# Kernel optimization log

Hardware: AMD Instinct MI355X
Metric: run time of the kernel (lower is better)

Reference implementation:

```python
import jax, jax.numpy as jnp
import numpy as np

SCALES = (16, 32, 64, 128)
P = 8
D = 1024
H = 16
DEPTH = 8
MLP = 4096
NCLS = 1000
PB = [(s // P) ** 2 for s in SCALES]            # [4, 16, 64, 256]
BLOCKS = [PB[0] + 1] + PB[1:]                    # [5, 16, 64, 256]
L = sum(BLOCKS)                                  # 341
PATCH_L = sum(PB)                                # 340
PD = P * P * 3                                   # 192
HD = D // H
EPS = 1e-6

# scale id per token (start token belongs to scale 0)
_SID = np.concatenate([np.full(n, k, dtype=np.int32) for k, n in enumerate(BLOCKS)])
# additive block-causal mask: token in scale q may attend to scales <= q
_ALLOW = _SID[None, :] <= _SID[:, None]
MASK = jnp.where(jnp.asarray(_ALLOW), 0.0, -1e30).astype(jnp.float32)  # [L, L]
SID = jnp.asarray(_SID)


def _ln(x):
    m = jnp.mean(x, axis=-1, keepdims=True)
    v = jnp.var(x, axis=-1, keepdims=True)
    return (x - m) / jnp.sqrt(v + EPS)


def _l2n(t):
    n = jnp.sqrt(jnp.sum(t * t, axis=-1, keepdims=True))
    return t / jnp.maximum(n, 1e-12)


def setup_inputs() -> dict:
    key = jax.random.key(0)
    ks = jax.random.split(key, 16)
    s = 0.02
    inp = {
        "patches": jax.random.normal(ks[0], (8, PATCH_L, PD), jnp.float32),
        "labels": jax.random.randint(ks[1], (8,), 0, NCLS),
        "W_patch": s * jax.random.normal(ks[2], (PD, D), jnp.float32),
        "b_patch": jnp.zeros((D,), jnp.float32),
        "pos": s * jax.random.normal(ks[3], (1, L, D), jnp.float32),
        "scale_emb": s * jax.random.normal(ks[4], (len(SCALES), D), jnp.float32),
        "class_emb": s * jax.random.normal(ks[5], (NCLS + 1, D), jnp.float32),
        "ada_W": s * jax.random.normal(ks[6], (DEPTH, D, 6 * D), jnp.float32),
        "ada_b": jnp.zeros((DEPTH, 6 * D), jnp.float32),
        "qkv_W": s * jax.random.normal(ks[7], (DEPTH, D, 3 * D), jnp.float32),
        "qkv_b": jnp.zeros((DEPTH, 3 * D), jnp.float32),
        "q_scale": jnp.zeros((DEPTH, 1, 1, H, 1), jnp.float32),  # log-scale per head
        "proj_W": s * jax.random.normal(ks[8], (DEPTH, D, D), jnp.float32),
        "proj_b": jnp.zeros((DEPTH, D), jnp.float32),
        "fc1_W": s * jax.random.normal(ks[9], (DEPTH, D, MLP), jnp.float32),
        "fc1_b": jnp.zeros((DEPTH, MLP), jnp.float32),
        "fc2_W": s * jax.random.normal(ks[10], (DEPTH, MLP, D), jnp.float32),
        "fc2_b": jnp.zeros((DEPTH, D), jnp.float32),
        "head_ada_W": s * jax.random.normal(ks[11], (D, 2 * D), jnp.float32),
        "head_ada_b": jnp.zeros((2 * D,), jnp.float32),
        "head_W": s * jax.random.normal(ks[12], (D, PD), jnp.float32),
        "head_b": jnp.zeros((PD,), jnp.float32),
    }
    return inp


def reference(patches, labels, W_patch, b_patch, pos, scale_emb, class_emb,
              ada_W, ada_b, qkv_W, qkv_b, q_scale, proj_W, proj_b,
              fc1_W, fc1_b, fc2_W, fc2_b, head_ada_W, head_ada_b, head_W, head_b):
    B = patches.shape[0]
    cond = class_emb[labels]                              # [B, D]
    tok = patches @ W_patch + b_patch                     # [B, PATCH_L, D]
    x = jnp.concatenate([cond[:, None, :], tok], axis=1)  # [B, L, D]
    x = x + pos + scale_emb[SID]

    for i in range(DEPTH):
        ada = jax.nn.silu(cond) @ ada_W[i] + ada_b[i]     # [B, 6D]
        g1, g2, s1, s2, sh1, sh2 = [a[:, None, :] for a in jnp.split(ada, 6, axis=-1)]
        # attention branch
        h = _ln(x) * (s1 + 1.0) + sh1
        qkv = (h @ qkv_W[i] + qkv_b[i]).reshape(B, L, 3, H, HD)
        q, k, v = qkv[:, :, 0], qkv[:, :, 1], qkv[:, :, 2]  # [B, L, H, HD]
        q = _l2n(q) * jnp.exp(q_scale[i])                  # attn_l2_norm
        k = _l2n(k)
        scores = jnp.einsum("bqhd,bkhd->bhqk", q, k) + MASK
        attn = jax.nn.softmax(scores, axis=-1)
        o = jnp.einsum("bhqk,bkhd->bqhd", attn, v).reshape(B, L, D)
        x = x + g1 * (o @ proj_W[i] + proj_b[i])
        # mlp branch
        h2 = _ln(x) * (s2 + 1.0) + sh2
        m = jax.nn.gelu(h2 @ fc1_W[i] + fc1_b[i]) @ fc2_W[i] + fc2_b[i]
        x = x + g2 * m

    ada = jax.nn.silu(cond) @ head_ada_W + head_ada_b     # [B, 2D]
    sc, sh = [a[:, None, :] for a in jnp.split(ada, 2, axis=-1)]
    x = _ln(x) * (sc + 1.0) + sh
    return x @ head_W + head_b                            # [B, L, PD]
```

## Files before the change

### kernel.cpp

```cpp
#include <hip/hip_runtime.h>

typedef unsigned short ushort_t;
typedef __bf16 bf16x8 __attribute__((ext_vector_type(8)));
typedef float f32x4 __attribute__((ext_vector_type(4)));

#define DEV __device__ __forceinline__

DEV ushort_t f2bf(float x) {
  union { float f; unsigned u; } v; v.f = x;
  unsigned r = v.u + 0x7FFFu + ((v.u >> 16) & 1u);
  return (ushort_t)(r >> 16);
}
DEV int sid_of(int l) { return l < 5 ? 0 : (l < 21 ? 1 : (l < 85 ? 2 : 3)); }
DEV float fast_tanh(float u) { return 1.0f - 2.0f / (__expf(2.0f * u) + 1.0f); }
DEV float gelu_f(float x) {
  float u = 0.7978845608028654f * (x + 0.044715f * x * x * x);
  return 0.5f * x * (1.0f + fast_tanh(u));
}
DEV float silu_f(float x) { return x / (1.0f + __expf(-x)); }
DEV f32x4 mfma16(bf16x8 a, bf16x8 b, f32x4 c) {
  return __builtin_amdgcn_mfma_f32_16x16x32_bf16(a, b, c, 0, 0, 0);
}
DEV void gload16(const void* src, void* dst) {
  __builtin_amdgcn_global_load_lds(
      (const __attribute__((address_space(1))) void*)(uintptr_t)src,
      (__attribute__((address_space(3))) void*)(uintptr_t)dst, 16, 0, 0);
}

__global__ __launch_bounds__(256) void k_cond_x0(
    const int* __restrict__ labels, const float* __restrict__ class_emb,
    const float* __restrict__ pos, const float* __restrict__ semb,
    float* __restrict__ cond, float* __restrict__ x) {
  int b = blockIdx.x, t = threadIdx.x;
  int lab = labels[b];
  float4 cv = *(const float4*)&class_emb[(size_t)lab * 1024 + t * 4];
  *(float4*)&cond[(size_t)b * 1024 + t * 4] = cv;
  float4 pv = *(const float4*)&pos[t * 4];
  float4 sv = *(const float4*)&semb[t * 4];
  float4 xv;
  xv.x = cv.x + pv.x + sv.x; xv.y = cv.y + pv.y + sv.y;
  xv.z = cv.z + pv.z + sv.z; xv.w = cv.w + pv.w + sv.w;
  *(float4*)&x[(size_t)b * 341 * 1024 + t * 4] = xv;
}

__global__ __launch_bounds__(256) void k_convert(const float* __restrict__ src,
                                                 ushort_t* __restrict__ dst, int n4) {
  int i = blockIdx.x * 256 + threadIdx.x;
  if (i < n4) {
    float4 v = *(const float4*)&src[(size_t)i * 4];
    uint2 pk;
    pk.x = (unsigned)f2bf(v.x) | ((unsigned)f2bf(v.y) << 16);
    pk.y = (unsigned)f2bf(v.z) | ((unsigned)f2bf(v.w) << 16);
    *(uint2*)&dst[(size_t)i * 4] = pk;
  }
}

__global__ __launch_bounds__(256) void k_transpose(const float* __restrict__ src,
                                                   ushort_t* __restrict__ dst, int K, int N) {
  __shared__ ushort_t tile[32][33];
  int z = blockIdx.z;
  src += (size_t)z * K * N;
  dst += (size_t)z * K * N;
  int k0 = blockIdx.y * 32, n0 = blockIdx.x * 32;
  int t = threadIdx.x;
  int r = t >> 3, c = (t & 7) * 4;
  float4 v = *(const float4*)&src[(size_t)(k0 + r) * N + n0 + c];
  tile[r][c] = f2bf(v.x); tile[r][c + 1] = f2bf(v.y);
  tile[r][c + 2] = f2bf(v.z); tile[r][c + 3] = f2bf(v.w);
  __syncthreads();
  ushort_t o0 = tile[c][r], o1 = tile[c + 1][r], o2 = tile[c + 2][r], o3 = tile[c + 3][r];
  uint2 pk;
  pk.x = (unsigned)o0 | ((unsigned)o1 << 16);
  pk.y = (unsigned)o2 | ((unsigned)o3 << 16);
  *(uint2*)&dst[(size_t)(n0 + r) * K + k0 + c] = pk;
}

__global__ __launch_bounds__(256) void k_ada(const float* __restrict__ cond,
    const float* __restrict__ ada_W, const float* __restrict__ ada_b,
    const float* __restrict__ hada_W, const float* __restrict__ hada_b,
    float* __restrict__ ada_out, float* __restrict__ hada_out) {
  int gy = blockIdx.y;
  bool head = (gy == 8);
  int Nw = head ? 2048 : 6144;
  int n0 = blockIdx.x * 64;
  if (n0 >= Nw) return;
  __shared__ float sc[8 * 1024];
  __shared__ float red[4][64][8];
  int t = threadIdx.x;
  for (int i = t; i < 2048; i += 256) {
    float4 cv = *(const float4*)&cond[(size_t)i * 4];
    float* d = &sc[i * 4];
    d[0] = silu_f(cv.x); d[1] = silu_f(cv.y); d[2] = silu_f(cv.z); d[3] = silu_f(cv.w);
  }
  __syncthreads();
  const float* W = head ? hada_W : ada_W + (size_t)gy * 1024 * 6144;
  const float* bs = head ? hada_b : ada_b + (size_t)gy * 6144;
  float* op = head ? hada_out : ada_out + (size_t)gy * 8 * 6144;
  int col = n0 + (t & 63), kq = t >> 6;
  float acc[8] = {0.f, 0.f, 0.f, 0.f, 0.f, 0.f, 0.f, 0.f};
  for (int k = kq * 256; k < kq * 256 + 256; ++k) {
    float wv = W[(size_t)k * Nw + col];
#pragma unroll
    for (int b2 = 0; b2 < 8; ++b2) acc[b2] += wv * sc[b2 * 1024 + k];
  }
#pragma unroll
  for (int b2 = 0; b2 < 8; ++b2) red[kq][t & 63][b2] = acc[b2];
  __syncthreads();
  if (t < 64) {
    int colc = n0 + t;
    float bias = bs[colc];
#pragma unroll
    for (int b2 = 0; b2 < 8; ++b2) {
      float v = red[0][t][b2] + red[1][t][b2] + red[2][t][b2] + red[3][t][b2] + bias;
      op[(size_t)b2 * Nw + colc] = v;
    }
  }
}

__global__ __launch_bounds__(256) void k_ln(const float* __restrict__ x,
    ushort_t* __restrict__ hout, const float* __restrict__ ada,
    int stride, int soff, int shoff) {
  int row = blockIdx.x, t = threadIdx.x;
  int b = row / 341;
  const float* xr = x + (size_t)row * 1024;
  float4 xv = *(const float4*)&xr[t * 4];
  float s = xv.x + xv.y + xv.z + xv.w;
  float ss = xv.x * xv.x + xv.y * xv.y + xv.z * xv.z + xv.w * xv.w;
#pragma unroll
  for (int off = 1; off < 64; off <<= 1) { s += __shfl_xor(s, off); ss += __shfl_xor(ss, off); }
  __shared__ float red[8];
  int w = t >> 6, lane = t & 63;
  if (lane == 0) { red[w] = s; red[w + 4] = ss; }
  __syncthreads();
  s = red[0] + red[1] + red[2] + red[3];
  ss = red[4] + red[5] + red[6] + red[7];
  float mean = s * (1.f / 1024.f);
  float var = ss * (1.f / 1024.f) - mean * mean;
  float rstd = rsqrtf(var + 1e-6f);
  const float* ar = ada + (size_t)b * stride;
  float xe[4] = {xv.x, xv.y, xv.z, xv.w};
  ushort_t tmp[4];
#pragma unroll
  for (int j = 0; j < 4; ++j) {
    int n = t * 4 + j;
    float val = (xe[j] - mean) * rstd * (1.f + ar[soff + n]) + ar[shoff + n];
    tmp[j] = f2bf(val);
  }
  uint2 pk;
  pk.x = (unsigned)tmp[0] | ((unsigned)tmp[1] << 16);
  pk.y = (unsigned)tmp[2] | ((unsigned)tmp[3] << 16);
  *(uint2*)&hout[(size_t)row * 1024 + t * 4] = pk;
}

__global__ __launch_bounds__(256) void k_comb_ln(
    const float* __restrict__ p, const float* __restrict__ bias,
    const float* __restrict__ adag, int goff,
    float* __restrict__ x, const float* __restrict__ adaln,
    int lnstride, int soff, int shoff,
    ushort_t* __restrict__ hout) {
  int row = blockIdx.x, t = threadIdx.x;
  int b = row / 341;
  int c = t * 4;
  float4 s4 = *(const float4*)&p[(size_t)row * 1024 + c];
  float4 q2 = *(const float4*)&p[(size_t)2728 * 1024 + (size_t)row * 1024 + c];
  s4.x += q2.x; s4.y += q2.y; s4.z += q2.z; s4.w += q2.w;
  float4 bv = *(const float4*)&bias[c];
  const float* gr = adag + (size_t)b * 6144 + goff + c;
  float4 xv = *(float4*)&x[(size_t)row * 1024 + c];
  xv.x += gr[0] * (s4.x + bv.x);
  xv.y += gr[1] * (s4.y + bv.y);
  xv.z += gr[2] * (s4.z + bv.z);
  xv.w += gr[3] * (s4.w + bv.w);
  *(float4*)&x[(size_t)row * 1024 + c] = xv;
  float sm = xv.x + xv.y + xv.z + xv.w;
  float ss = xv.x * xv.x + xv.y * xv.y + xv.z * xv.z + xv.w * xv.w;
#pragma unroll
  for (int off = 1; off < 64; off <<= 1) { sm += __shfl_xor(sm, off); ss += __shfl_xor(ss, off); }
  __shared__ float red[8];
  int w = t >> 6, lane = t & 63;
  if (lane == 0) { red[w] = sm; red[w + 4] = ss; }
  __syncthreads();
  sm = red[0] + red[1] + red[2] + red[3];
  ss = red[4] + red[5] + red[6] + red[7];
  float mean = sm * (1.f / 1024.f);
  float var = ss * (1.f / 1024.f) - mean * mean;
  float rstd = rsqrtf(var + 1e-6f);
  const float* ar = adaln + (size_t)b * lnstride;
  float xe[4] = {xv.x, xv.y, xv.z, xv.w};
  ushort_t tmp[4];
#pragma unroll
  for (int j = 0; j < 4; ++j) {
    int n = c + j;
    float val = (xe[j] - mean) * rstd * (1.f + ar[soff + n]) + ar[shoff + n];
    tmp[j] = f2bf(val);
  }
  uint2 pk;
  pk.x = (unsigned)tmp[0] | ((unsigned)tmp[1] << 16);
  pk.y = (unsigned)tmp[2] | ((unsigned)tmp[3] << 16);
  *(uint2*)&hout[(size_t)row * 1024 + c] = pk;
}

template <int EPI, int BM>
__global__ __launch_bounds__(256, 3) void k_gemm(
    const ushort_t* __restrict__ A, const ushort_t* __restrict__ Bt,
    const float* __restrict__ bias, float* __restrict__ fout,
    ushort_t* __restrict__ bfout, const float* __restrict__ aux,
    float* __restrict__ xres, const float* __restrict__ pos,
    const float* __restrict__ semb, int M, int N, int K, int KS) {
  constexpr int NI = (BM == 128) ? 4 : 2;
  constexpr int WNB = (BM == 128) ? 64 : 32;
  __shared__ ushort_t aT[3][BM * 32];
  __shared__ ushort_t bT[3][128 * 32];
  int tid = threadIdx.x;
  int lane = tid & 63, w = tid >> 6;
  int WR = (BM == 128) ? (w >> 1) : 0;
  int WC = (BM == 128) ? (w & 1) : w;

  int gx = gridDim.x;
  int nwg = gx * gridDim.y;
  int orig = blockIdx.y * gx + blockIdx.x;
  int q = nwg >> 3, r8 = nwg & 7;
  int xcd = orig & 7, idx = orig >> 3;
  int lin = (xcd < r8 ? xcd * (q + 1) : r8 * (q + 1) + (xcd - r8) * q) + idx;
  int bx = lin % gx, by = lin / gx;

  int m0 = by * BM, n0 = bx * 128;
  int kbase = blockIdx.z * KS;
  f32x4 acc[4][NI];
#pragma unroll
  for (int i = 0; i < 4; ++i)
#pragma unroll
    for (int j = 0; j < NI; ++j) acc[i][j] = (f32x4){0.f, 0.f, 0.f, 0.f};

  int lrow = lane & 15;
  int csw = (lrow >> 1) & 3;
  int coff = ((lane >> 4) ^ csw) * 8;

  int s_row0 = tid >> 2, s_u = tid & 3;
  int s_c = s_u ^ ((s_row0 >> 1) & 3);
  int aR0 = m0 + s_row0; if (aR0 > M - 1) aR0 = M - 1;
  int bR0 = n0 + s_row0; if (bR0 > N - 1) bR0 = N - 1;
  int aR1 = m0 + s_row0 + 64; if (aR1 > M - 1) aR1 = M - 1;
  int bR1 = n0 + s_row0 + 64; if (bR1 > N - 1) bR1 = N - 1;
  const ushort_t* aSrc0 = A + (size_t)aR0 * K + kbase + s_c * 8;
  const ushort_t* aSrc1 = A + (size_t)aR1 * K + kbase + s_c * 8;
  const ushort_t* bSrc0 = Bt + (size_t)bR0 * K + kbase + s_c * 8;
  const ushort_t* bSrc1 = Bt + (size_t)bR1 * K + kbase + s_c * 8;
  int slot0 = w * 512, slot1 = 2048 + w * 512;

  int nsteps = KS >> 5;
  auto STAGE = [&](int k0, int buf) {
    gload16(aSrc0 + k0, &aT[buf][slot0]);
    if constexpr (BM == 128) gload16(aSrc1 + k0, &aT[buf][slot1]);
    gload16(bSrc0 + k0, &bT[buf][slot0]);
    gload16(bSrc1 + k0, &bT[buf][slot1]);
  };

  STAGE(0, 0);
  int cur = 0;
  for (int s = 0; s < nsteps; ++s) {
    int nb = cur + 1; if (nb == 3) nb = 0;
    int kn = (s + 1 < nsteps) ? ((s + 1) << 5) : 0;
    STAGE(kn, nb);
    if constexpr (BM == 128)
      asm volatile("s_waitcnt vmcnt(4)" ::: "memory");
    else
      asm volatile("s_waitcnt vmcnt(3)" ::: "memory");
    __builtin_amdgcn_sched_barrier(0);
    __builtin_amdgcn_s_barrier();
    __builtin_amdgcn_sched_barrier(0);
    bf16x8 af[4], bb[NI];
#pragma unroll
    for (int mi = 0; mi < 4; ++mi)
      af[mi] = *(const bf16x8*)&aT[cur][(WR * 64 + mi * 16 + lrow) * 32 + coff];
#pragma unroll
    for (int ni = 0; ni < NI; ++ni)
      bb[ni] = *(const bf16x8*)&bT[cur][(WC * WNB + ni * 16 + lrow) * 32 + coff];
#pragma unroll
    for (int mi = 0; mi < 4; ++mi)
#pragma unroll
      for (int ni = 0; ni < NI; ++ni)
        acc[mi][ni] = mfma16(af[mi], bb[ni], acc[mi][ni]);
    cur = nb;
  }

  if constexpr (EPI == 6) {
    int nb = n0 + WC * 64;
    int gh = nb >> 6;
    float qse = (gh < 16) ? __expf(aux[gh]) : 1.0f;
    bool dn = gh < 32;
#pragma unroll
    for (int mi = 0; mi < 4; ++mi) {
#pragma unroll
      for (int r = 0; r < 4; ++r) {
        float vv[4]; float ss = 0.f;
#pragma unroll
        for (int ni = 0; ni < 4; ++ni) {
          vv[ni] = acc[mi][ni][r] + bias[nb + ni * 16 + lrow];
          ss += vv[ni] * vv[ni];
        }
        if (dn) {
          ss += __shfl_xor(ss, 1); ss += __shfl_xor(ss, 2);
          ss += __shfl_xor(ss, 4); ss += __shfl_xor(ss, 8);
          float rn = qse / fmaxf(sqrtf(ss), 1e-12f);
#pragma unroll
          for (int ni = 0; ni < 4; ++ni) vv[ni] *= rn;
        }
        int gm = m0 + WR * 64 + mi * 16 + (lane >> 4) * 4 + r;
        if (gm < M) {
#pragma unroll
          for (int ni = 0; ni < 4; ++ni)
            bfout[(size_t)gm * N + nb + ni * 16 + lrow] = f2bf(vv[ni]);
        }
      }
    }
  } else {
#pragma unroll
    for (int mi = 0; mi < 4; ++mi) {
#pragma unroll
      for (int ni = 0; ni < NI; ++ni) {
#pragma unroll
        for (int r = 0; r < 4; ++r) {
          int gm = m0 + WR * 64 + mi * 16 + (lane >> 4) * 4 + r;
          int gn = n0 + WC * WNB + ni * 16 + lrow;
          if (gm >= M || gn >= N) continue;
          if constexpr (EPI == 7) {
            fout[(size_t)blockIdx.z * M * N + (size_t)gm * N + gn] = acc[mi][ni][r];
          } else {
            float v = acc[mi][ni][r] + bias[gn];
            if constexpr (EPI == 1) {
              int b = gm / 341;
              xres[(size_t)gm * 1024 + gn] += aux[(size_t)b * 6144 + gn] * v;
            } else if constexpr (EPI == 2) {
              bfout[(size_t)gm * N + gn] = f2bf(gelu_f(v));
            } else if constexpr (EPI == 4) {
              int b = gm / 340, l = gm % 340 + 1;
              float val = v + pos[(size_t)l * 1024 + gn] + semb[(size_t)sid_of(l) * 1024 + gn];
              xres[((size_t)(b * 341 + l)) * 1024 + gn] = val;
            }
          }
        }
      }
    }
  }
}

__global__ __launch_bounds__(256) void k_comb_head(const float* __restrict__ p,
    const float* __restrict__ bias, float* __restrict__ out, int nsplit) {
  int row = blockIdx.x, t = threadIdx.x;
  const int N = 192;
  size_t stride = (size_t)2728 * N;
  if (t < 48) {
    int c = t * 4;
    float4 s = *(const float4*)&p[(size_t)row * N + c];
    for (int sp = 1; sp < nsplit; ++sp) {
      float4 qq = *(const float4*)&p[sp * stride + (size_t)row * N + c];
      s.x += qq.x; s.y += qq.y; s.z += qq.z; s.w += qq.w;
    }
    float4 bv = *(const float4*)&bias[c];
    s.x += bv.x; s.y += bv.y; s.z += bv.z; s.w += bv.w;
    *(float4*)&out[(size_t)row * N + c] = s;
  }
}

__global__ __launch_bounds__(256) void k_attn(
    const ushort_t* __restrict__ qkv, ushort_t* __restrict__ o) {
  int qt = blockIdx.x, h = blockIdx.y, b = blockIdx.z;
  int t = threadIdx.x, lane = t & 63, w = t >> 6;
  int q0 = qt * 64;
  __shared__ ushort_t qT[64 * 72], kT[64 * 72], vS[64 * 72], vT[64 * 72];
  __shared__ ushort_t pT[4][16 * 72];
#pragma unroll
  for (int i = 0; i < 2; ++i) {
    int vid = t + 256 * i;
    int row = vid >> 3, seg = (vid & 7) * 8;
    int l = q0 + row; if (l > 340) l = 340;
    uint4 v = *(const uint4*)&qkv[((size_t)(b * 341 + l)) * 3072 + h * 64 + seg];
    *(uint4*)&qT[row * 72 + seg] = v;
  }
  int lrow = lane & 15, lk8 = (lane >> 4) * 8;
  int sq[4];
  float mrun[4], lsum[4];
  f32x4 accO[4];
#pragma unroll
  for (int r = 0; r < 4; ++r) {
    int lq = q0 + w * 16 + (lane >> 4) * 4 + r;
    sq[r] = sid_of(lq < 341 ? lq : 340);
    mrun[r] = -1e30f;
    lsum[r] = 0.f;
  }
#pragma unroll
  for (int d = 0; d < 4; ++d) accO[d] = (f32x4){0.f, 0.f, 0.f, 0.f};
  int nch = (qt == 0) ? 2 : 6;
  int vd = t >> 2, vlseg = (t & 3) * 16;
  for (int c = 0; c < nch; ++c) {
    __syncthreads();
#pragma unroll
    for (int i = 0; i < 2; ++i) {
      int vid = t + 256 * i;
      int row = vid >> 3, seg = (vid & 7) * 8;
      int l = c * 64 + row; if (l > 340) l = 340;
      size_t base = ((size_t)(b * 341 + l)) * 3072 + h * 64 + seg;
      uint4 kv = *(const uint4*)&qkv[base + 1024];
      uint4 vv = *(const uint4*)&qkv[base + 2048];
      *(uint4*)&kT[row * 72 + seg] = kv;
      *(uint4*)&vS[row * 72 + seg] = vv;
    }
    __syncthreads();
    ushort_t tmp[16];
#pragma unroll
    for (int j = 0; j < 16; ++j) tmp[j] = vS[(vlseg + j) * 72 + vd];
    f32x4 sf[4];
#pragma unroll
    for (int nf = 0; nf < 4; ++nf) sf[nf] = (f32x4){0.f, 0.f, 0.f, 0.f};
    __builtin_amdgcn_s_setprio(1);
#pragma unroll
    for (int ks = 0; ks < 2; ++ks) {
      bf16x8 aq = *(const bf16x8*)&qT[(w * 16 + lrow) * 72 + ks * 32 + lk8];
#pragma unroll
      for (int nf = 0; nf < 4; ++nf) {
        bf16x8 bk = *(const bf16x8*)&kT[(nf * 16 + lrow) * 72 + ks * 32 + lk8];
        sf[nf] = mfma16(aq, bk, sf[nf]);
      }
    }
    __builtin_amdgcn_s_setprio(0);
#pragma unroll
    for (int nf = 0; nf < 4; ++nf) {
      int lk = c * 64 + nf * 16 + lrow;
      int sk = lk < 341 ? sid_of(lk) : 9;
#pragma unroll
      for (int r = 0; r < 4; ++r)
        if (sk > sq[r]) sf[nf][r] = -1e30f;
    }
    float rs[4];
#pragma unroll
    for (int r = 0; r < 4; ++r) {
      float m = sf[0][r];
      m = fmaxf(m, sf[1][r]); m = fmaxf(m, sf[2][r]); m = fmaxf(m, sf[3][r]);
#pragma unroll
      for (int off = 1; off < 16; off <<= 1) m = fmaxf(m, __shfl_xor(m, off));
      float mn = fmaxf(mrun[r], m);
      float scl = __expf(mrun[r] - mn);
      mrun[r] = mn;
      lsum[r] *= scl;
#pragma unroll
      for (int d = 0; d < 4; ++d) accO[d][r] *= scl;
      rs[r] = 0.f;
    }
    ushort_t* pw = &pT[w][0];
#pragma unroll
    for (int nf = 0; nf < 4; ++nf) {
#pragma unroll
      for (int r = 0; r < 4; ++r) {
        float p = __expf(sf[nf][r] - mrun[r]);
        rs[r] += p;
        pw[((lane >> 4) * 4 + r) * 72 + nf * 16 + lrow] = f2bf(p);
      }
    }
#pragma unroll
    for (int r = 0; r < 4; ++r) {
      float sum = rs[r];
#pragma unroll
      for (int off = 1; off < 16; off <<= 1) sum += __shfl_xor(sum, off);
      lsum[r] += sum;
    }
    {
      uint4 s0, s1;
      s0.x = (unsigned)tmp[0] | ((unsigned)tmp[1] << 16);
      s0.y = (unsigned)tmp[2] | ((unsigned)tmp[3] << 16);
      s0.z = (unsigned)tmp[4] | ((unsigned)tmp[5] << 16);
      s0.w = (unsigned)tmp[6] | ((unsigned)tmp[7] << 16);
      s1.x = (unsigned)tmp[8] | ((unsigned)tmp[9] << 16);
      s1.y = (unsigned)tmp[10] | ((unsigned)tmp[11] << 16);
      s1.z = (unsigned)tmp[12] | ((unsigned)tmp[13] << 16);
      s1.w = (unsigned)tmp[14] | ((unsigned)tmp[15] << 16);
      *(uint4*)&vT[vd * 72 + vlseg] = s0;
      *(uint4*)&vT[vd * 72 + vlseg + 8] = s1;
    }
    __syncthreads();
    __builtin_amdgcn_s_setprio(1);
#pragma unroll
    for (int ks = 0; ks < 2; ++ks) {
      bf16x8 ap = *(const bf16x8*)&pw[lrow * 72 + ks * 32 + lk8];
#pragma unroll
      for (int d = 0; d < 4; ++d) {
        bf16x8 bv = *(const bf16x8*)&vT[(d * 16 + lrow) * 72 + ks * 32 + lk8];
        accO[d] = mfma16(ap, bv, accO[d]);
      }
    }
    __builtin_amdgcn_s_setprio(0);
  }
#pragma unroll
  for (int d = 0; d < 4; ++d) {
#pragma unroll
    for (int r = 0; r < 4; ++r) {
      int lq = q0 + w * 16 + (lane >> 4) * 4 + r;
      if (lq < 341) {
        float ov = accO[d][r] / fmaxf(lsum[r], 1e-30f);
        o[((size_t)(b * 341 + lq)) * 1024 + h * 64 + d * 16 + lrow] = f2bf(ov);
      }
    }
  }
}

extern "C" void kernel_launch(void* const* d_in, const int* in_sizes, int n_in,
                              void* d_out, int out_size, void* d_ws, size_t ws_size,
                              hipStream_t stream) {
  const float* patches   = (const float*)d_in[0];
  const int*   labels    = (const int*)d_in[1];
  const float* W_patch   = (const float*)d_in[2];
  const float* b_patch   = (const float*)d_in[3];
  const float* pos       = (const float*)d_in[4];
  const float* scale_emb = (const float*)d_in[5];
  const float* class_emb = (const float*)d_in[6];
  const float* ada_W     = (const float*)d_in[7];
  const float* ada_b     = (const float*)d_in[8];
  const float* qkv_W     = (const float*)d_in[9];
  const float* qkv_b     = (const float*)d_in[10];
  const float* q_scale   = (const float*)d_in[11];
  const float* proj_W    = (const float*)d_in[12];
  const float* proj_b    = (const float*)d_in[13];
  const float* fc1_W     = (const float*)d_in[14];
  const float* fc1_b     = (const float*)d_in[15];
  const float* fc2_W     = (const float*)d_in[16];
  const float* fc2_b     = (const float*)d_in[17];
  const float* hada_W    = (const float*)d_in[18];
  const float* hada_b    = (const float*)d_in[19];
  const float* head_W    = (const float*)d_in[20];
  const float* head_b    = (const float*)d_in[21];
  (void)in_sizes; (void)n_in; (void)out_size; (void)ws_size;

  char* wsb = (char*)d_ws;
  size_t off = 0;
  auto alloc = [&](size_t bytes) -> void* {
    void* p = wsb + off;
    off = (off + bytes + 255) & ~(size_t)255;
    return p;
  };

  float*    f_cond   = (float*)alloc(8 * 1024 * 4);
  float*    f_ada    = (float*)alloc((size_t)8 * 8 * 6144 * 4);
  float*    f_hada   = (float*)alloc(8 * 2048 * 4);
  float*    f_x      = (float*)alloc((size_t)2728 * 1024 * 4);
  ushort_t* u_h      = (ushort_t*)alloc((size_t)2728 * 1024 * 2);
  ushort_t* u_qkv    = (ushort_t*)alloc((size_t)2728 * 3072 * 2);
  ushort_t* u_o      = (ushort_t*)alloc((size_t)2728 * 1024 * 2);
  ushort_t* u_mid    = (ushort_t*)alloc((size_t)2728 * 4096 * 2);
  float*    f_part   = (float*)alloc((size_t)2 * 2728 * 1024 * 4);
  ushort_t* u_patch  = (ushort_t*)alloc((size_t)2720 * 192 * 2);
  ushort_t* u_qkvt   = (ushort_t*)alloc((size_t)8 * 3072 * 1024 * 2);
  ushort_t* u_projt  = (ushort_t*)alloc((size_t)8 * 1024 * 1024 * 2);
  ushort_t* u_fc1t   = (ushort_t*)alloc((size_t)8 * 4096 * 1024 * 2);
  ushort_t* u_fc2t   = (ushort_t*)alloc((size_t)8 * 1024 * 4096 * 2);
  ushort_t* u_wpt    = (ushort_t*)alloc((size_t)1024 * 192 * 2);
  ushort_t* u_wht    = (ushort_t*)alloc((size_t)192 * 1024 * 2);

  const int MT = 22;
  const int MT64 = 43;

  k_cond_x0<<<8, 256, 0, stream>>>(labels, class_emb, pos, scale_emb, f_cond, f_x);
  k_transpose<<<dim3(32, 6, 1), 256, 0, stream>>>(W_patch, u_wpt, 192, 1024);
  k_transpose<<<dim3(6, 32, 1), 256, 0, stream>>>(head_W, u_wht, 1024, 192);
  k_convert<<<510, 256, 0, stream>>>(patches, u_patch, 130560);
  k_ada<<<dim3(96, 9), 256, 0, stream>>>(f_cond, ada_W, ada_b, hada_W, hada_b, f_ada, f_hada);
  k_transpose<<<dim3(96, 32, 8), 256, 0, stream>>>(qkv_W, u_qkvt, 1024, 3072);
  k_transpose<<<dim3(32, 32, 8), 256, 0, stream>>>(proj_W, u_projt, 1024, 1024);
  k_transpose<<<dim3(128, 32, 8), 256, 0, stream>>>(fc1_W, u_fc1t, 1024, 4096);
  k_transpose<<<dim3(32, 128, 8), 256, 0, stream>>>(fc2_W, u_fc2t, 4096, 1024);

  k_gemm<4, 128><<<dim3(8, MT), 256, 0, stream>>>(u_patch, u_wpt, b_patch, nullptr, nullptr,
                                                  nullptr, f_x, pos, scale_emb, 2720, 1024, 192, 192);
  k_ln<<<2728, 256, 0, stream>>>(f_x, u_h, f_ada, 6144, 2048, 4096);

  for (int i = 0; i < 8; ++i) {
    const float* adaL = f_ada + (size_t)i * 8 * 6144;
    k_gemm<6, 128><<<dim3(24, MT), 256, 0, stream>>>(u_h, u_qkvt + (size_t)i * 3072 * 1024,
                                                     qkv_b + (size_t)i * 3072, nullptr, u_qkv,
                                                     q_scale + (size_t)i * 16, nullptr, nullptr,
                                                     nullptr, 2728, 3072, 1024, 1024);
    k_attn<<<dim3(6, 16, 8), 256, 0, stream>>>(u_qkv, u_o);
    k_gemm<1, 64><<<dim3(8, MT64, 1), 256, 0, stream>>>(u_o, u_projt + (size_t)i * 1024 * 1024,
                                                        proj_b + (size_t)i * 1024, nullptr,
                                                        nullptr, adaL, f_x, nullptr, nullptr,
                                                        2728, 1024, 1024, 1024);
    k_ln<<<2728, 256, 0, stream>>>(f_x, u_h, adaL, 6144, 3072, 5120);
    k_gemm<2, 128><<<dim3(32, MT), 256, 0, stream>>>(u_h, u_fc1t + (size_t)i * 4096 * 1024,
                                                     fc1_b + (size_t)i * 4096, nullptr,
                                                     u_mid, nullptr, nullptr, nullptr, nullptr,
                                                     2728, 4096, 1024, 1024);
    k_gemm<7, 64><<<dim3(8, MT64, 2), 256, 0, stream>>>(u_mid, u_fc2t + (size_t)i * 4096 * 1024,
                                                        nullptr, f_part, nullptr, nullptr,
                                                        nullptr, nullptr, nullptr,
                                                        2728, 1024, 4096, 2048);
    if (i < 7) {
      k_comb_ln<<<2728, 256, 0, stream>>>(f_part, fc2_b + (size_t)i * 1024, adaL, 1024,
                                          f_x, f_ada + (size_t)(i + 1) * 8 * 6144,
                                          6144, 2048, 4096, u_h);
    } else {
      k_comb_ln<<<2728, 256, 0, stream>>>(f_part, fc2_b + (size_t)i * 1024, adaL, 1024,
                                          f_x, f_hada, 2048, 0, 1024, u_h);
    }
  }

  k_gemm<7, 64><<<dim3(2, MT64, 4), 256, 0, stream>>>(u_h, u_wht, nullptr, f_part, nullptr,
                                                      nullptr, nullptr, nullptr, nullptr,
                                                      2728, 192, 1024, 256);
  k_comb_head<<<2728, 256, 0, stream>>>(f_part, head_b, (float*)d_out, 4);
}
```

Before: 1.779 ms.

## Pretranspose V into a global buffer and add lazy softmax rescaling

New measurement: 1.786 ms. Within noise of the previous version (+0.4%).

```diff
diff --git a/kernel.cpp b/kernel.cpp
--- a/kernel.cpp
+++ b/kernel.cpp
@@ -363,12 +363,47 @@
   }
 }
 
+__global__ __launch_bounds__(256) void k_vt(const ushort_t* __restrict__ qkv,
+                                            ushort_t* __restrict__ vt) {
+  int c = blockIdx.x, h = blockIdx.y, b = blockIdx.z;
+  __shared__ ushort_t tile[64 * 72];
+  int t = threadIdx.x;
+#pragma unroll
+  for (int i = 0; i < 2; ++i) {
+    int vid = t + 256 * i;
+    int row = vid >> 3, seg = (vid & 7) * 8;
+    int l = c * 64 + row; if (l > 340) l = 340;
+    uint4 v = *(const uint4*)&qkv[((size_t)(b * 341 + l)) * 3072 + 2048 + h * 64 + seg];
+    *(uint4*)&tile[row * 72 + seg] = v;
+  }
+  __syncthreads();
+  int d = t >> 2, lseg = (t & 3) * 16;
+  ushort_t tmp[16];
+#pragma unroll
+  for (int j = 0; j < 16; ++j) tmp[j] = tile[(lseg + j) * 72 + d];
+  size_t bh = (size_t)(b * 16 + h);
+  ushort_t* dp = vt + (bh * 64 + d) * 384 + c * 64 + lseg;
+  uint4 s0, s1;
+  s0.x = (unsigned)tmp[0] | ((unsigned)tmp[1] << 16);
+  s0.y = (unsigned)tmp[2] | ((unsigned)tmp[3] << 16);
+  s0.z = (unsigned)tmp[4] | ((unsigned)tmp[5] << 16);
+  s0.w = (unsigned)tmp[6] | ((unsigned)tmp[7] << 16);
+  s1.x = (unsigned)tmp[8] | ((unsigned)tmp[9] << 16);
+  s1.y = (unsigned)tmp[10] | ((unsigned)tmp[11] << 16);
+  s1.z = (unsigned)tmp[12] | ((unsigned)tmp[13] << 16);
+  s1.w = (unsigned)tmp[14] | ((unsigned)tmp[15] << 16);
+  *(uint4*)dp = s0;
+  *(uint4*)(dp + 8) = s1;
+}
+
 __global__ __launch_bounds__(256) void k_attn(
-    const ushort_t* __restrict__ qkv, ushort_t* __restrict__ o) {
+    const ushort_t* __restrict__ qkv, const ushort_t* __restrict__ vtg,
+    ushort_t* __restrict__ o) {
   int qt = blockIdx.x, h = blockIdx.y, b = blockIdx.z;
   int t = threadIdx.x, lane = t & 63, w = t >> 6;
   int q0 = qt * 64;
-  __shared__ ushort_t qT[64 * 72], kT[64 * 72], vS[64 * 72], vT[64 * 72];
+  size_t bh64 = (size_t)(b * 16 + h) * 64;
+  __shared__ ushort_t qT[64 * 72], kT[64 * 72], vT[64 * 72];
   __shared__ ushort_t pT[4][16 * 72];
 #pragma unroll
   for (int i = 0; i < 2; ++i) {
@@ -392,7 +427,6 @@
 #pragma unroll
   for (int d = 0; d < 4; ++d) accO[d] = (f32x4){0.f, 0.f, 0.f, 0.f};
   int nch = (qt == 0) ? 2 : 6;
-  int vd = t >> 2, vlseg = (t & 3) * 16;
   for (int c = 0; c < nch; ++c) {
     __syncthreads();
 #pragma unroll
@@ -400,16 +434,12 @@
       int vid = t + 256 * i;
       int row = vid >> 3, seg = (vid & 7) * 8;
       int l = c * 64 + row; if (l > 340) l = 340;
-      size_t base = ((size_t)(b * 341 + l)) * 3072 + h * 64 + seg;
-      uint4 kv = *(const uint4*)&qkv[base + 1024];
-      uint4 vv = *(const uint4*)&qkv[base + 2048];
+      uint4 kv = *(const uint4*)&qkv[((size_t)(b * 341 + l)) * 3072 + 1024 + h * 64 + seg];
       *(uint4*)&kT[row * 72 + seg] = kv;
-      *(uint4*)&vS[row * 72 + seg] = vv;
+      uint4 vv = *(const uint4*)&vtg[(bh64 + row) * 384 + c * 64 + seg];
+      *(uint4*)&vT[row * 72 + seg] = vv;
     }
     __syncthreads();
-    ushort_t tmp[16];
-#pragma unroll
-    for (int j = 0; j < 16; ++j) tmp[j] = vS[(vlseg + j) * 72 + vd];
     f32x4 sf[4];
 #pragma unroll
     for (int nf = 0; nf < 4; ++nf) sf[nf] = (f32x4){0.f, 0.f, 0.f, 0.f};
@@ -439,12 +469,13 @@
       m = fmaxf(m, sf[1][r]); m = fmaxf(m, sf[2][r]); m = fmaxf(m, sf[3][r]);
 #pragma unroll
       for (int off = 1; off < 16; off <<= 1) m = fmaxf(m, __shfl_xor(m, off));
-      float mn = fmaxf(mrun[r], m);
-      float scl = __expf(mrun[r] - mn);
-      mrun[r] = mn;
-      lsum[r] *= scl;
-#pragma unroll
-      for (int d = 0; d < 4; ++d) accO[d][r] *= scl;
+      if (m > mrun[r] + 8.0f) {
+        float scl = __expf(mrun[r] - m);
+        mrun[r] = m;
+        lsum[r] *= scl;
+#pragma unroll
+        for (int d = 0; d < 4; ++d) accO[d][r] *= scl;
+      }
       rs[r] = 0.f;
     }
     ushort_t* pw = &pT[w][0];
@@ -464,20 +495,6 @@
       for (int off = 1; off < 16; off <<= 1) sum += __shfl_xor(sum, off);
       lsum[r] += sum;
     }
-    {
-      uint4 s0, s1;
-      s0.x = (unsigned)tmp[0] | ((unsigned)tmp[1] << 16);
-      s0.y = (unsigned)tmp[2] | ((unsigned)tmp[3] << 16);
-      s0.z = (unsigned)tmp[4] | ((unsigned)tmp[5] << 16);
-      s0.w = (unsigned)tmp[6] | ((unsigned)tmp[7] << 16);
-      s1.x = (unsigned)tmp[8] | ((unsigned)tmp[9] << 16);
-      s1.y = (unsigned)tmp[10] | ((unsigned)tmp[11] << 16);
-      s1.z = (unsigned)tmp[12] | ((unsigned)tmp[13] << 16);
-      s1.w = (unsigned)tmp[14] | ((unsigned)tmp[15] << 16);
-      *(uint4*)&vT[vd * 72 + vlseg] = s0;
-      *(uint4*)&vT[vd * 72 + vlseg + 8] = s1;
-    }
-    __syncthreads();
     __builtin_amdgcn_s_setprio(1);
 #pragma unroll
     for (int ks = 0; ks < 2; ++ks) {
@@ -544,6 +561,7 @@
   float*    f_x      = (float*)alloc((size_t)2728 * 1024 * 4);
   ushort_t* u_h      = (ushort_t*)alloc((size_t)2728 * 1024 * 2);
   ushort_t* u_qkv    = (ushort_t*)alloc((size_t)2728 * 3072 * 2);
+  ushort_t* u_vt     = (ushort_t*)alloc((size_t)128 * 64 * 384 * 2);
   ushort_t* u_o      = (ushort_t*)alloc((size_t)2728 * 1024 * 2);
   ushort_t* u_mid    = (ushort_t*)alloc((size_t)2728 * 4096 * 2);
   float*    f_part   = (float*)alloc((size_t)2 * 2728 * 1024 * 4);
@@ -578,7 +596,8 @@
                                                      qkv_b + (size_t)i * 3072, nullptr, u_qkv,
                                                      q_scale + (size_t)i * 16, nullptr, nullptr,
                                                      nullptr, 2728, 3072, 1024, 1024);
-    k_attn<<<dim3(6, 16, 8), 256, 0, stream>>>(u_qkv, u_o);
+    k_vt<<<dim3(6, 16, 8), 256, 0, stream>>>(u_qkv, u_vt);
+    k_attn<<<dim3(6, 16, 8), 256, 0, stream>>>(u_qkv, u_vt, u_o);
     k_gemm<1, 64><<<dim3(8, MT64, 1), 256, 0, stream>>>(u_o, u_projt + (size_t)i * 1024 * 1024,
                                                         proj_b + (size_t)i * 1024, nullptr,
                                                         nullptr, adaL, f_x, nullptr, nullptr,
```
